# Optimization experiments

Measured on AMD Instinct MI355X. Metric: run time of the kernel, lower is better.

The kernel has to match this reference:

```python
import jax, jax.numpy as jnp
import numpy as np
import math

B, N, S, H = 2, 4, 1024, 512
HEADS = 8
HEAD = H // HEADS
SCALE_BASE = 512  # xpos default scale_base
EPS = 1e-5        # GroupNorm eps


def _xpos_tables(seq_len, d):
    """Precompute xpos sin/cos/scale tables, duplicate-interleaved to width d."""
    half = d // 2
    scale_vec = (np.arange(0, d, 2) + 0.4 * d) / (1.4 * d)          # (half,)
    power = np.arange(seq_len)[:, None] / SCALE_BASE                # (S,1)
    scale = scale_vec[None, :] ** power                             # (S,half)
    inv_freq = 1.0 / (10000.0 ** (np.arange(half) / half))
    ang = np.arange(seq_len)[:, None] * inv_freq[None, :]           # (S,half)
    dup = lambda m: np.repeat(m, 2, axis=-1)                        # duplicate_interleave
    return (jnp.asarray(dup(np.sin(ang)), jnp.float32),
            jnp.asarray(dup(np.cos(ang)), jnp.float32),
            jnp.asarray(dup(scale), jnp.float32))


def _rot2(x):
    # rotate_every_two: (x0,x1,x2,x3,...) -> (-x1,x0,-x3,x2,...)
    x1 = x[..., ::2]
    x2 = x[..., 1::2]
    return jnp.stack([-x2, x1], axis=-1).reshape(x.shape)


def _decay_masks(seq_len, heads):
    # gammas from MultiScaleRetention.__init__; D[g,i,j] = gamma_g**(i-j) if i>=j else 0
    g = 1.0 - np.exp(np.linspace(math.log(1.0 / 32), math.log(1.0 / 512), heads))
    idx = np.arange(seq_len)
    diff = idx[:, None] - idx[None, :]
    D = np.where(diff >= 0, g[:, None, None] ** np.maximum(diff, 0), 0.0)
    return jnp.asarray(D, jnp.float32)


def setup_inputs():
    key = jax.random.key(0)
    ks = jax.random.split(key, 6)
    X = jax.random.normal(ks[0], (B, N, S, H), jnp.float32)
    W_Q = jax.random.normal(ks[1], (HEADS, H, HEAD), jnp.float32) / H
    W_K = jax.random.normal(ks[2], (HEADS, H, HEAD), jnp.float32) / H
    W_V = jax.random.normal(ks[3], (HEADS, H, HEAD), jnp.float32) / H
    W_G = jax.random.normal(ks[4], (H, H), jnp.float32) / H
    W_O = jax.random.normal(ks[5], (H, H), jnp.float32) / H
    gn_weight = jnp.ones((H,), jnp.float32)
    gn_bias = jnp.zeros((H,), jnp.float32)
    return {"X": X, "W_Q": W_Q, "W_K": W_K, "W_V": W_V,
            "W_G": W_G, "W_O": W_O, "gn_weight": gn_weight, "gn_bias": gn_bias}


def reference(X, W_Q, W_K, W_V, W_G, W_O, gn_weight, gn_bias):
    heads, _, head = W_Q.shape
    b, n, s, h = X.shape
    sin, cos, scale = _xpos_tables(s, head)   # each (s, head)
    D = _decay_masks(s, heads)                # (g, s, s)

    # per-head projections, all heads at once
    Q = jnp.einsum('bnsh,ghd->gbnsd', X, W_Q)
    K = jnp.einsum('bnsh,ghd->gbnsd', X, W_K)
    V = jnp.einsum('bnsh,ghd->gbnsd', X, W_V)
    # xpos rotary: Q upscaled, K downscaled
    Q = (Q * cos + _rot2(Q) * sin) * scale
    K = (K * cos + _rot2(K) * sin) / scale

    # decay-masked retention: (Q K^T * D) V per head
    scores = jnp.einsum('gbnsd,gbntd->gbnst', Q, K) * D[:, None, None]
    Y = jnp.einsum('gbnst,gbntd->gbnsd', scores, V)   # (g,b,n,s,head)

    # GroupNorm(heads groups over v_dim channels): normalize each head's channels
    mean = Y.mean(-1, keepdims=True)
    var = Y.var(-1, keepdims=True)
    Yn = (Y - mean) * jax.lax.rsqrt(var + EPS)
    Yn = Yn * gn_weight.reshape(heads, 1, 1, 1, head) + gn_bias.reshape(heads, 1, 1, 1, head)

    # concat heads on feature dim -> (b,n,s,v_dim)
    Ycat = jnp.moveaxis(Yn, 0, 3).reshape(b, n, s, heads * head)

    gate = X @ W_G
    gate = gate * jax.nn.sigmoid(gate)        # swish
    return (gate * Ycat) @ W_O
```

## Files before the change

### kernel.cpp

```cpp
#include <hip/hip_runtime.h>
#include <hip/hip_bf16.h>
#include <math.h>


typedef __attribute__((ext_vector_type(8))) short bf16x8;
typedef __attribute__((ext_vector_type(4))) float f32x4;

#define MFMA16(a, b, c) __builtin_amdgcn_mfma_f32_16x16x32_bf16(a, b, c, 0, 0, 0)
#define BAR() __builtin_amdgcn_s_barrier()
#define WAITV(n) asm volatile("s_waitcnt vmcnt(" #n ")" ::: "memory")
#define LGKM0() asm volatile("s_waitcnt lgkmcnt(0)" ::: "memory")
#define CVTPK(a, b) ({ unsigned _r;                                   \
  asm("v_cvt_pk_bf16_f32 %0, %1, %2" : "=v"(_r) : "v"(a), "v"(b));    \
  _r; })

__device__ __forceinline__ unsigned short f2bf(float f) {
  union { float f; unsigned u; } x; x.f = f;
  unsigned r = x.u + 0x7FFFu + ((x.u >> 16) & 1u);
  return (unsigned short)(r >> 16);
}
__device__ __forceinline__ float bf2f(unsigned short b) {
  union { unsigned u; float f; } x; x.u = ((unsigned)b) << 16;
  return x.f;
}

__device__ __forceinline__ void gload_chunk(const unsigned short* gtile, size_t gstride,
                                            unsigned short* lds, int chunk, int lane) {
  int r = (chunk << 3) + (lane >> 3);
  int colel = ((lane & 7) ^ (lane >> 3)) << 3;
  const unsigned short* gp = gtile + (size_t)r * gstride + colel;
  __builtin_amdgcn_global_load_lds(
      (const __attribute__((address_space(1))) unsigned int*)gp,
      (__attribute__((address_space(3))) unsigned int*)((char*)lds + (chunk << 10)),
      16, 0, 0);
}

__device__ __forceinline__ bf16x8 frag64(const unsigned short* lds, int row, int colel) {
  return *(const bf16x8*)((const char*)lds + row * 128 + ((colel * 2) ^ ((row & 7) << 4)));
}


__global__ void k_prep(const float* __restrict__ X, const float* __restrict__ WQ,
                       const float* __restrict__ WK, const float* __restrict__ WV,
                       const float* __restrict__ WG, const float* __restrict__ WO,
                       unsigned short* __restrict__ Xb, unsigned short* __restrict__ Wcat,
                       unsigned short* __restrict__ WoT,
                       float2* __restrict__ qtab, float2* __restrict__ ktab) {
  int b = blockIdx.x, tid = threadIdx.x;
  if (b < 4096) {
    int idx = b * 256 + tid;
    float4 v = ((const float4*)X)[idx];
    uint2 o;
    o.x = CVTPK(v.x, v.y);
    o.y = CVTPK(v.z, v.w);
    ((uint2*)Xb)[idx] = o;
    return;
  }
  if (b < 4416) {
    __shared__ float Ls[64][68];
    const float* src;
    unsigned short* dst;
    size_t src_ld, dst_rowbase, dst_colbase;
    int b2;
    if (b < 4288) {
      b2 = b - 4096;
      const float* W = (b2 < 64) ? WQ : (b2 < 128 ? WK : WV);
      int cls = (b2 < 64) ? 0 : (b2 < 128 ? 1 : 2);
      int gg = (b2 & 63) >> 3, kt = b2 & 7;
      src = W + ((size_t)gg * 512 + kt * 64) * 64;
      src_ld = 64;
      dst = Wcat;
      dst_rowbase = (size_t)cls * 512 + gg * 64;
      dst_colbase = (size_t)kt * 64;
    } else if (b < 4352) {
      b2 = b - 4288;
      int kt = b2 >> 3, nt = b2 & 7;
      src = WG + (size_t)(kt * 64) * 512 + nt * 64;
      src_ld = 512;
      dst = Wcat;
      dst_rowbase = 1536 + (size_t)nt * 64;
      dst_colbase = (size_t)kt * 64;
    } else {
      b2 = b - 4352;
      int kt = b2 >> 3, nt = b2 & 7;
      src = WO + (size_t)(kt * 64) * 512 + nt * 64;
      src_ld = 512;
      dst = WoT;
      dst_rowbase = (size_t)nt * 64;
      dst_colbase = (size_t)kt * 64;
    }
#pragma unroll
    for (int i = 0; i < 4; ++i) {
      int e = i * 256 + tid;
      int r = e >> 4, c4 = e & 15;
      float4 v = *(const float4*)(src + (size_t)r * src_ld + c4 * 4);
      *(float4*)&Ls[r][c4 * 4] = v;
    }
    __syncthreads();
    int d = tid >> 2, kp = (tid & 3) * 16;
    unsigned short tmp[16];
#pragma unroll
    for (int k = 0; k < 16; ++k) tmp[k] = f2bf(Ls[kp + k][d]);
    size_t orow = (dst_rowbase + d) * 512 + dst_colbase + kp;
    *(bf16x8*)(dst + orow) = *(bf16x8*)&tmp[0];
    *(bf16x8*)(dst + orow + 8) = *(bf16x8*)&tmp[8];
    return;
  }
  {
    int idx = (b - 4416) * 256 + tid;
    int s = idx >> 5, i = idx & 31;
    float invf = exp2f(-(float)i * (13.2877123795f / 32.0f));
    float ang = (float)s * invf;
    float sn = sinf(ang), cs = cosf(ang);
    float sv = (2.f * i + 25.6f) / 89.6f;
    float sc = exp2f(log2f(sv) * (float)s * (1.f / 512.f));
    qtab[idx] = make_float2(cs * sc, sn * sc);
    ktab[idx] = make_float2(cs / sc, sn / sc);
  }
}


__launch_bounds__(512, 2)
__global__ void k_proj(const unsigned short* __restrict__ Xb, const unsigned short* __restrict__ Wt,
                       const float2* __restrict__ qtab, const float2* __restrict__ ktab,
                       unsigned short* __restrict__ Qb, unsigned short* __restrict__ Kb,
                       unsigned short* __restrict__ Vb, unsigned short* __restrict__ Gb) {
  __shared__ __attribute__((aligned(16))) unsigned short As[2][256 * 64];
  __shared__ __attribute__((aligned(16))) unsigned short Bs[2][256 * 64];
  const int tid = threadIdx.x, lane = tid & 63, wid = tid >> 6;
  const int wr = wid >> 2, wc = wid & 3;
  const int cb = blockIdx.x, rb = blockIdx.y;

  f32x4 acc[8][4] = {};
  const int kc = (lane >> 4) * 8;
  const unsigned short* Ag = Xb + (size_t)(rb * 256) * 512;
  const unsigned short* Bg = Wt + (size_t)(cb * 256) * 512;

#define PSTAGE(kt, buf)                                             \
  {                                                                 \
    _Pragma("unroll") for (int i = 0; i < 4; ++i) {                 \
      gload_chunk(Ag + (kt) * 64, 512, As[buf], wid * 4 + i, lane); \
      gload_chunk(Bg + (kt) * 64, 512, Bs[buf], wid * 4 + i, lane); \
    }                                                               \
  }

  PSTAGE(0, 0);
  for (int kt = 0; kt < 8; ++kt) {
    const int cur = kt & 1;
    if (kt < 7) {
      PSTAGE(kt + 1, cur ^ 1);
      WAITV(8);
    } else {
      WAITV(0);
    }
    BAR();
#pragma unroll
    for (int ks = 0; ks < 2; ++ks) {
      bf16x8 a[8], b[4];
#pragma unroll
      for (int mi = 0; mi < 8; ++mi) a[mi] = frag64(As[cur], wr * 128 + mi * 16 + (lane & 15), ks * 32 + kc);
#pragma unroll
      for (int ni = 0; ni < 4; ++ni) b[ni] = frag64(Bs[cur], wc * 64 + ni * 16 + (lane & 15), ks * 32 + kc);
#pragma unroll
      for (int mi = 0; mi < 8; ++mi)
#pragma unroll
        for (int ni = 0; ni < 4; ++ni)
          acc[mi][ni] = MFMA16(a[mi], b[ni], acc[mi][ni]);
    }
    LGKM0();
    BAR();
  }
#undef PSTAGE

  float* patch = (float*)As + wid * (16 * 68);
  const int rr = lane >> 2;
  const int c0 = (lane & 3) * 16;
  const int row0 = rb * 256 + wr * 128;
  const int colc = (cb & 1) * 256 + wc * 64;
  const int cls = cb >> 1;
  const int i0 = c0 >> 1;

#pragma unroll
  for (int mi = 0; mi < 8; ++mi) {
#pragma unroll
    for (int ni = 0; ni < 4; ++ni)
#pragma unroll
      for (int r = 0; r < 4; ++r)
        patch[((lane >> 4) * 4 + r) * 68 + ni * 16 + (lane & 15)] = acc[mi][ni][r];
    float v[16];
#pragma unroll
    for (int q = 0; q < 4; ++q) {
      float4 t = *(float4*)&patch[rr * 68 + c0 + q * 4];
      v[q * 4 + 0] = t.x; v[q * 4 + 1] = t.y; v[q * 4 + 2] = t.z; v[q * 4 + 3] = t.w;
    }
    int grow = row0 + mi * 16 + rr;
    int s = grow & 1023;
    unsigned out[8];
    if (cls <= 1) {
      const float2* tab = (cls == 0) ? qtab : ktab;
#pragma unroll
      for (int p = 0; p < 8; ++p) {
        float2 t = tab[s * 32 + i0 + p];
        float e = v[2 * p], o = v[2 * p + 1];
        out[p] = CVTPK(e * t.x - o * t.y, o * t.x + e * t.y);
      }
    } else if (cls == 2) {
#pragma unroll
      for (int p = 0; p < 8; ++p) out[p] = CVTPK(v[2 * p], v[2 * p + 1]);
    } else {
#pragma unroll
      for (int p = 0; p < 8; ++p) {
        float e = v[2 * p], o = v[2 * p + 1];
        e = e / (1.f + __expf(-e));
        o = o / (1.f + __expf(-o));
        out[p] = CVTPK(e, o);
      }
    }
    unsigned short* dst = (cls == 0) ? Qb : (cls == 1) ? Kb : (cls == 2) ? Vb : Gb;
    *(uint4*)(dst + (size_t)grow * 512 + colc + c0) = *(uint4*)&out[0];
    *(uint4*)(dst + (size_t)grow * 512 + colc + c0 + 8) = *(uint4*)&out[4];
  }
}


__launch_bounds__(256)
__global__ void k_ret(const unsigned short* __restrict__ Qb, const unsigned short* __restrict__ Kb,
                      const unsigned short* __restrict__ Vb, const unsigned short* __restrict__ Gb,
                      const float* __restrict__ gnw, const float* __restrict__ gnb,
                      unsigned short* __restrict__ Ab) {
  __shared__ __attribute__((aligned(16))) unsigned short Qs[128 * 64];
  __shared__ __attribute__((aligned(16))) unsigned short Ks[2][64 * 64];
  __shared__ __attribute__((aligned(16))) unsigned short Vs[2][64][72];
  __shared__ __attribute__((aligned(16))) unsigned short Ss[128][72];
  const int u = blockIdx.x;
  const int v = u & 255;
  const int hi = u >> 8;
  const int sraw = v & 7, g = (v >> 3) & 7;
  const int bn = (v >> 6) + (hi ? 4 : 0);
  const int sblk = hi ? 7 - sraw : sraw;
  const int tid = threadIdx.x, lane = tid & 63, w = tid >> 6;

  const float lg0 = logf(1.f / 32.f), lg1 = logf(1.f / 512.f);
  const float gam = 1.f - expf(lg0 + g * (lg1 - lg0) / 7.f);
  const float l2g = log2f(gam);

  const int s0 = sblk * 128;
  const size_t seqbase = (size_t)bn * 1024;
  const int kc = (lane >> 4) * 8;
  const int ntt = 2 * sblk + 2;

  float cf[16];
#pragma unroll
  for (int ti = 0; ti < 4; ++ti)
#pragma unroll
    for (int r = 0; r < 4; ++r)
      cf[ti * 4 + r] = exp2f(l2g * (float)(-(ti * 16 + (lane >> 4) * 4 + r)));
  const int sRow[2] = { w * 32 + (lane & 15), w * 32 + 16 + (lane & 15) };

  const int t0p = (tid >> 3) * 2;
  const int c0v = (tid & 7) * 8;
  const unsigned short* Vg = Vb + seqbase * 512 + g * 64 + c0v;

#define KSTAGE(t, buf)                                                        \
  {                                                                           \
    gload_chunk(Kb + (seqbase + (t) * 64) * 512 + g * 64, 512, Ks[buf], w * 2 + 0, lane); \
    gload_chunk(Kb + (seqbase + (t) * 64) * 512 + g * 64, 512, Ks[buf], w * 2 + 1, lane); \
  }
#define VLOAD(t, r0, r1)                                                      \
  {                                                                           \
    r0 = *(const bf16x8*)(Vg + (size_t)((t) * 64 + t0p) * 512);               \
    r1 = *(const bf16x8*)(Vg + (size_t)((t) * 64 + t0p + 1) * 512);           \
  }
#define VWRITE(buf, r0, r1)                                                   \
  {                                                                           \
    _Pragma("unroll") for (int j = 0; j < 8; ++j) {                           \
      int d = c0v + j;                                                        \
      ushort2 pp; pp.x = (unsigned short)r0[j]; pp.y = (unsigned short)r1[j]; \
      *(ushort2*)&Vs[buf][d][t0p ^ (d & 0x38)] = pp;                          \
    }                                                                         \
  }

  bf16x8 vA0, vA1, vB0, vB1;

  const unsigned short* Qg = Qb + (seqbase + s0) * 512 + g * 64;
#pragma unroll
  for (int i = 0; i < 4; ++i) gload_chunk(Qg, 512, Qs, w * 4 + i, lane);
  KSTAGE(0, 0);
  VLOAD(0, vA0, vA1);
  WAITV(0);
  VWRITE(0, vA0, vA1);
  KSTAGE(1, 1);
  VLOAD(1, vB0, vB1);
  LGKM0();
  BAR();

  bf16x8 qreg[2][2];
#pragma unroll
  for (int ks = 0; ks < 2; ++ks)
#pragma unroll
    for (int si = 0; si < 2; ++si)
      qreg[ks][si] = frag64(Qs, w * 32 + si * 16 + (lane & 15), ks * 32 + kc);

  f32x4 accY[2][4] = {};

  auto body = [&](int tt, int cur, bf16x8& w0, bf16x8& w1, bf16x8& l0, bf16x8& l1) {
    const int t0 = tt * 64;
    f32x4 accSt[4][2] = {};
#pragma unroll
    for (int ks = 0; ks < 2; ++ks) {
      bf16x8 kf[4];
#pragma unroll
      for (int ti = 0; ti < 4; ++ti) kf[ti] = frag64(Ks[cur], ti * 16 + (lane & 15), ks * 32 + kc);
#pragma unroll
      for (int ti = 0; ti < 4; ++ti)
#pragma unroll
        for (int si = 0; si < 2; ++si)
          accSt[ti][si] = MFMA16(kf[ti], qreg[ks][si], accSt[ti][si]);
    }

    float rf[2];
    rf[0] = exp2f(l2g * (float)(s0 + sRow[0] - t0));
    rf[1] = exp2f(l2g * (float)(s0 + sRow[1] - t0));
    if (tt >= 2 * sblk) {
#pragma unroll
      for (int ti = 0; ti < 4; ++ti)
#pragma unroll
        for (int si = 0; si < 2; ++si) {
          int tb = ti * 16 + (lane >> 4) * 4;
          float p[4];
#pragma unroll
          for (int r = 0; r < 4; ++r) {
            int diff = (s0 + sRow[si]) - (t0 + tb + r);
            float dv = (diff >= 0) ? rf[si] * cf[ti * 4 + r] : 0.f;
            p[r] = accSt[ti][si][r] * dv;
          }
          uint2 pk; pk.x = CVTPK(p[0], p[1]); pk.y = CVTPK(p[2], p[3]);
          *(uint2*)&Ss[sRow[si]][tb] = pk;
        }
    } else {
#pragma unroll
      for (int ti = 0; ti < 4; ++ti)
#pragma unroll
        for (int si = 0; si < 2; ++si) {
          int tb = ti * 16 + (lane >> 4) * 4;
          uint2 pk;
          pk.x = CVTPK(accSt[ti][si][0] * rf[si] * cf[ti * 4 + 0],
                       accSt[ti][si][1] * rf[si] * cf[ti * 4 + 1]);
          pk.y = CVTPK(accSt[ti][si][2] * rf[si] * cf[ti * 4 + 2],
                       accSt[ti][si][3] * rf[si] * cf[ti * 4 + 3]);
          *(uint2*)&Ss[sRow[si]][tb] = pk;
        }
    }

#pragma unroll
    for (int ks = 0; ks < 2; ++ks) {
      bf16x8 af[2], vf[4];
#pragma unroll
      for (int mi = 0; mi < 2; ++mi) af[mi] = *(const bf16x8*)&Ss[sRow[mi]][ks * 32 + kc];
#pragma unroll
      for (int ni = 0; ni < 4; ++ni) {
        int d = ni * 16 + (lane & 15);
        vf[ni] = *(const bf16x8*)&Vs[cur][d][(ks * 32 + kc) ^ (d & 0x38)];
      }
#pragma unroll
      for (int mi = 0; mi < 2; ++mi)
#pragma unroll
        for (int ni = 0; ni < 4; ++ni)
          accY[mi][ni] = MFMA16(af[mi], vf[ni], accY[mi][ni]);
    }

    LGKM0();
    BAR();
    if (tt + 1 < ntt) {
      WAITV(0);
      VWRITE(cur ^ 1, w0, w1);
      if (tt + 2 < ntt) {
        KSTAGE(tt + 2, cur);
        VLOAD(tt + 2, l0, l1);
      }
      LGKM0();
      BAR();
    }
  };

  for (int tt = 0; tt < ntt; tt += 2) {
    body(tt, 0, vB0, vB1, vA0, vA1);
    body(tt + 1, 1, vA0, vA1, vB0, vB1);
  }

  float gw[4], gbv[4];
#pragma unroll
  for (int ni = 0; ni < 4; ++ni) {
    int d = ni * 16 + (lane & 15);
    gw[ni] = gnw[g * 64 + d];
    gbv[ni] = gnb[g * 64 + d];
  }
#pragma unroll
  for (int mi = 0; mi < 2; ++mi)
#pragma unroll
    for (int r = 0; r < 4; ++r) {
      float sm = 0.f, sq = 0.f;
#pragma unroll
      for (int ni = 0; ni < 4; ++ni) { float vv = accY[mi][ni][r]; sm += vv; sq += vv * vv; }
#pragma unroll
      for (int off = 1; off < 16; off <<= 1) { sm += __shfl_xor(sm, off); sq += __shfl_xor(sq, off); }
      float mean = sm * (1.f / 64.f);
      float var = sq * (1.f / 64.f) - mean * mean;
      float rstd = rsqrtf(var + 1e-5f);
      int row = w * 32 + mi * 16 + (lane >> 4) * 4 + r;
      size_t grow = (seqbase + s0 + row) * 512 + g * 64;
#pragma unroll
      for (int ni = 0; ni < 4; ++ni) {
        int d = ni * 16 + (lane & 15);
        float vv = (accY[mi][ni][r] - mean) * rstd * gw[ni] + gbv[ni];
        float gate = bf2f(Gb[grow + d]);
        Ab[grow + d] = f2bf(vv * gate);
      }
    }
#undef KSTAGE
#undef VLOAD
#undef VWRITE
}


__launch_bounds__(256)
__global__ void k_out(const unsigned short* __restrict__ Ab, const unsigned short* __restrict__ Wt,
                      float* __restrict__ out) {
  __shared__ __attribute__((aligned(16))) unsigned short As[2][128 * 64];
  __shared__ __attribute__((aligned(16))) unsigned short Bs[2][64 * 64];
  const int tid = threadIdx.x, lane = tid & 63, wid = tid >> 6;
  const int wr = wid >> 1, wc = wid & 1;
  const int cb = blockIdx.x, rb = blockIdx.y;

  f32x4 acc[4][2] = {};
  const int kc = (lane >> 4) * 8;
  const unsigned short* Ag = Ab + (size_t)(rb * 128) * 512;
  const unsigned short* Bg = Wt + (size_t)(cb * 64) * 512;

#define OSTAGE(kt, buf)                                                  \
  {                                                                      \
    _Pragma("unroll") for (int i = 0; i < 4; ++i)                        \
        gload_chunk(Ag + (kt) * 64, 512, As[buf], wid * 4 + i, lane);    \
    _Pragma("unroll") for (int i = 0; i < 2; ++i)                        \
        gload_chunk(Bg + (kt) * 64, 512, Bs[buf], wid * 2 + i, lane);    \
  }

  OSTAGE(0, 0);
  for (int kt = 0; kt < 8; ++kt) {
    const int cur = kt & 1;
    if (kt < 7) {
      OSTAGE(kt + 1, cur ^ 1);
      WAITV(6);
    } else {
      WAITV(0);
    }
    BAR();
#pragma unroll
    for (int ks = 0; ks < 2; ++ks) {
      bf16x8 a[4], b[2];
#pragma unroll
      for (int mi = 0; mi < 4; ++mi) a[mi] = frag64(As[cur], wr * 64 + mi * 16 + (lane & 15), ks * 32 + kc);
#pragma unroll
      for (int ni = 0; ni < 2; ++ni) b[ni] = frag64(Bs[cur], wc * 32 + ni * 16 + (lane & 15), ks * 32 + kc);
#pragma unroll
      for (int mi = 0; mi < 4; ++mi)
#pragma unroll
        for (int ni = 0; ni < 2; ++ni)
          acc[mi][ni] = MFMA16(a[mi], b[ni], acc[mi][ni]);
    }
    LGKM0();
    BAR();
  }
#undef OSTAGE

  const int row0 = rb * 128 + wr * 64;
  const int col0 = cb * 64 + wc * 32;
#pragma unroll
  for (int mi = 0; mi < 4; ++mi)
#pragma unroll
    for (int ni = 0; ni < 2; ++ni) {
      int col = col0 + ni * 16 + (lane & 15);
#pragma unroll
      for (int r = 0; r < 4; ++r) {
        int row = row0 + mi * 16 + (lane >> 4) * 4 + r;
        out[(size_t)row * 512 + col] = acc[mi][ni][r];
      }
    }
}


extern "C" void kernel_launch(void* const* d_in, const int* in_sizes, int n_in,
                              void* d_out, int out_size, void* d_ws, size_t ws_size,
                              hipStream_t stream) {
  const float* X   = (const float*)d_in[0];
  const float* WQ  = (const float*)d_in[1];
  const float* WK  = (const float*)d_in[2];
  const float* WV  = (const float*)d_in[3];
  const float* WG  = (const float*)d_in[4];
  const float* WO  = (const float*)d_in[5];
  const float* gnw = (const float*)d_in[6];
  const float* gnb = (const float*)d_in[7];
  float* out = (float*)d_out;

  char* ws = (char*)d_ws;
  const size_t SZ_BUF = (size_t)8192 * 512 * 2;
  unsigned short* Xb   = (unsigned short*)(ws);
  unsigned short* Qb   = (unsigned short*)(ws + SZ_BUF);
  unsigned short* Kb   = (unsigned short*)(ws + 2 * SZ_BUF);
  unsigned short* Vb   = (unsigned short*)(ws + 3 * SZ_BUF);
  unsigned short* Gb   = (unsigned short*)(ws + 4 * SZ_BUF);
  unsigned short* Ab   = (unsigned short*)(ws + 5 * SZ_BUF);
  unsigned short* Wcat = (unsigned short*)(ws + 6 * SZ_BUF);
  unsigned short* WoT  = (unsigned short*)(ws + 6 * SZ_BUF + 2097152);
  float2* qtab = (float2*)(ws + 6 * SZ_BUF + 2097152 + 524288);
  float2* ktab = qtab + 32768;

  k_prep<<<4544, 256, 0, stream>>>(X, WQ, WK, WV, WG, WO, Xb, Wcat, WoT, qtab, ktab);
  k_proj<<<dim3(8, 32), 512, 0, stream>>>(Xb, Wcat, qtab, ktab, Qb, Kb, Vb, Gb);
  k_ret<<<512, 256, 0, stream>>>(Qb, Kb, Vb, Gb, gnw, gnb, Ab);
  k_out<<<dim3(8, 64), 256, 0, stream>>>(Ab, WoT, out);
}
```

Baseline: 149.8 us.

## Fuse X fp32-to-bf16 conversion into projection GEMM A-tile loading

```diff
diff --git a/kernel.cpp b/kernel.cpp
--- a/kernel.cpp
+++ b/kernel.cpp
@@ -40,40 +40,28 @@
 }
 
 
-__global__ void k_prep(const float* __restrict__ X, const float* __restrict__ WQ,
+__global__ void k_prep(const float* __restrict__ WQ,
                        const float* __restrict__ WK, const float* __restrict__ WV,
                        const float* __restrict__ WG, const float* __restrict__ WO,
-                       unsigned short* __restrict__ Xb, unsigned short* __restrict__ Wcat,
-                       unsigned short* __restrict__ WoT,
+                       unsigned short* __restrict__ Wcat, unsigned short* __restrict__ WoT,
                        float2* __restrict__ qtab, float2* __restrict__ ktab) {
   int b = blockIdx.x, tid = threadIdx.x;
-  if (b < 4096) {
-    int idx = b * 256 + tid;
-    float4 v = ((const float4*)X)[idx];
-    uint2 o;
-    o.x = CVTPK(v.x, v.y);
-    o.y = CVTPK(v.z, v.w);
-    ((uint2*)Xb)[idx] = o;
-    return;
-  }
-  if (b < 4416) {
+  if (b < 320) {
     __shared__ float Ls[64][68];
     const float* src;
     unsigned short* dst;
     size_t src_ld, dst_rowbase, dst_colbase;
-    int b2;
-    if (b < 4288) {
-      b2 = b - 4096;
-      const float* W = (b2 < 64) ? WQ : (b2 < 128 ? WK : WV);
-      int cls = (b2 < 64) ? 0 : (b2 < 128 ? 1 : 2);
-      int gg = (b2 & 63) >> 3, kt = b2 & 7;
+    if (b < 192) {
+      const float* W = (b < 64) ? WQ : (b < 128 ? WK : WV);
+      int cls = (b < 64) ? 0 : (b < 128 ? 1 : 2);
+      int gg = (b & 63) >> 3, kt = b & 7;
       src = W + ((size_t)gg * 512 + kt * 64) * 64;
       src_ld = 64;
       dst = Wcat;
       dst_rowbase = (size_t)cls * 512 + gg * 64;
       dst_colbase = (size_t)kt * 64;
-    } else if (b < 4352) {
-      b2 = b - 4288;
+    } else if (b < 256) {
+      int b2 = b - 192;
       int kt = b2 >> 3, nt = b2 & 7;
       src = WG + (size_t)(kt * 64) * 512 + nt * 64;
       src_ld = 512;
@@ -81,7 +69,7 @@
       dst_rowbase = 1536 + (size_t)nt * 64;
       dst_colbase = (size_t)kt * 64;
     } else {
-      b2 = b - 4352;
+      int b2 = b - 256;
       int kt = b2 >> 3, nt = b2 & 7;
       src = WO + (size_t)(kt * 64) * 512 + nt * 64;
       src_ld = 512;
@@ -107,7 +95,7 @@
     return;
   }
   {
-    int idx = (b - 4416) * 256 + tid;
+    int idx = (b - 320) * 256 + tid;
     int s = idx >> 5, i = idx & 31;
     float invf = exp2f(-(float)i * (13.2877123795f / 32.0f));
     float ang = (float)s * invf;
@@ -121,7 +109,7 @@
 
 
 __launch_bounds__(512, 2)
-__global__ void k_proj(const unsigned short* __restrict__ Xb, const unsigned short* __restrict__ Wt,
+__global__ void k_proj(const float* __restrict__ X, const unsigned short* __restrict__ Wt,
                        const float2* __restrict__ qtab, const float2* __restrict__ ktab,
                        unsigned short* __restrict__ Qb, unsigned short* __restrict__ Kb,
                        unsigned short* __restrict__ Vb, unsigned short* __restrict__ Gb) {
@@ -133,27 +121,41 @@
 
   f32x4 acc[8][4] = {};
   const int kc = (lane >> 4) * 8;
-  const unsigned short* Ag = Xb + (size_t)(rb * 256) * 512;
+  const float* Agf = X + (size_t)(rb * 256) * 512;
   const unsigned short* Bg = Wt + (size_t)(cb * 256) * 512;
 
-#define PSTAGE(kt, buf)                                             \
-  {                                                                 \
-    _Pragma("unroll") for (int i = 0; i < 4; ++i) {                 \
-      gload_chunk(Ag + (kt) * 64, 512, As[buf], wid * 4 + i, lane); \
-      gload_chunk(Bg + (kt) * 64, 512, Bs[buf], wid * 4 + i, lane); \
-    }                                                               \
-  }
-
-  PSTAGE(0, 0);
+  float4 rA[8];
+  const int ar = tid >> 1;
+  const int acs = (tid & 1) * 32;
+
+#define ALOAD(kt)                                                          \
+  { _Pragma("unroll") for (int q = 0; q < 8; ++q)                          \
+      rA[q] = *(const float4*)(Agf + (size_t)ar * 512 + (kt) * 64 + acs + q * 4); }
+#define AWRITE(buf)                                                        \
+  { _Pragma("unroll") for (int j = 0; j < 4; ++j) {                        \
+      uint4 wv;                                                            \
+      wv.x = CVTPK(rA[2 * j].x, rA[2 * j].y);                              \
+      wv.y = CVTPK(rA[2 * j].z, rA[2 * j].w);                              \
+      wv.z = CVTPK(rA[2 * j + 1].x, rA[2 * j + 1].y);                      \
+      wv.w = CVTPK(rA[2 * j + 1].z, rA[2 * j + 1].w);                      \
+      *(uint4*)((char*)As[buf] + ar * 128 +                                \
+                ((acs * 2 + j * 16) ^ ((ar & 7) << 4))) = wv;              \
+    } }
+#define BSTAGE(kt, buf)                                                    \
+  { _Pragma("unroll") for (int i = 0; i < 4; ++i)                          \
+      gload_chunk(Bg + (kt) * 64, 512, Bs[buf], wid * 4 + i, lane); }
+
+  ALOAD(0);
+  BSTAGE(0, 0);
+  WAITV(0);
+  AWRITE(0);
+  BSTAGE(1, 1);
+  ALOAD(1);
+  LGKM0();
+  BAR();
+
   for (int kt = 0; kt < 8; ++kt) {
     const int cur = kt & 1;
-    if (kt < 7) {
-      PSTAGE(kt + 1, cur ^ 1);
-      WAITV(8);
-    } else {
-      WAITV(0);
-    }
-    BAR();
 #pragma unroll
     for (int ks = 0; ks < 2; ++ks) {
       bf16x8 a[8], b[4];
@@ -169,8 +171,17 @@
     }
     LGKM0();
     BAR();
-  }
-#undef PSTAGE
+    if (kt < 7) {
+      WAITV(0);
+      AWRITE(cur ^ 1);
+      if (kt < 6) { BSTAGE(kt + 2, cur); ALOAD(kt + 2); }
+      LGKM0();
+      BAR();
+    }
+  }
+#undef ALOAD
+#undef AWRITE
+#undef BSTAGE
 
   float* patch = (float*)As + wid * (16 * 68);
   const int rr = lane >> 2;
@@ -504,7 +515,6 @@
 
   char* ws = (char*)d_ws;
   const size_t SZ_BUF = (size_t)8192 * 512 * 2;
-  unsigned short* Xb   = (unsigned short*)(ws);
   unsigned short* Qb   = (unsigned short*)(ws + SZ_BUF);
   unsigned short* Kb   = (unsigned short*)(ws + 2 * SZ_BUF);
   unsigned short* Vb   = (unsigned short*)(ws + 3 * SZ_BUF);
@@ -515,8 +525,8 @@
   float2* qtab = (float2*)(ws + 6 * SZ_BUF + 2097152 + 524288);
   float2* ktab = qtab + 32768;
 
-  k_prep<<<4544, 256, 0, stream>>>(X, WQ, WK, WV, WG, WO, Xb, Wcat, WoT, qtab, ktab);
-  k_proj<<<dim3(8, 32), 512, 0, stream>>>(Xb, Wcat, qtab, ktab, Qb, Kb, Vb, Gb);
+  k_prep<<<448, 256, 0, stream>>>(WQ, WK, WV, WG, WO, Wcat, WoT, qtab, ktab);
+  k_proj<<<dim3(8, 32), 512, 0, stream>>>(X, Wcat, qtab, ktab, Qb, Kb, Vb, Gb);
   k_ret<<<512, 256, 0, stream>>>(Qb, Kb, Vb, Gb, gnw, gnb, Ab);
   k_out<<<dim3(8, 64), 256, 0, stream>>>(Ab, WoT, out);
 }
```

New measurement: 159.5 us. 1.06x slower.
